# Kernel tuning notes

Measured on AMD Instinct MI355X. Metric: run time of the kernel, lower is better.

## Reference

```python
import jax, jax.numpy as jnp
import numpy as np
import math

# dims (match init_kwargs / input_specs)
T, B, S = 2048, 8, 512
D, H, DFF, NQ, W = 512, 8, 2048, 10, 16
EPS = 1e-5
NEG = -1e30


def _ln(x, g, b):
    mu = jnp.mean(x, axis=-1, keepdims=True)
    var = jnp.mean((x - mu) ** 2, axis=-1, keepdims=True)
    return (x - mu) * jax.lax.rsqrt(var + EPS) * g + b


def setup_inputs() -> dict:
    key = jax.random.key(0)
    ks = jax.random.split(key, 10)
    f = lambda k, shape, s=0.02: jax.random.normal(k, shape, jnp.float32) * s
    return {
        'tgt': jax.random.normal(ks[0], (T, B, D), jnp.float32),
        'memory': jax.random.normal(ks[1], (S, B, D), jnp.float32),
        'queries': f(ks[2], (NQ, D), 1.0 / math.sqrt(D)),
        'wk': f(ks[3], (NQ, 1), 1.0 / math.sqrt(NQ)),
        'in_proj_w': f(ks[4], (3 * D, D)),
        'in_proj_b': jnp.zeros((3 * D,), jnp.float32),
        'out_proj_w': f(ks[5], (D, D)),
        'out_proj_b': jnp.zeros((D,), jnp.float32),
        'lin1_w': f(ks[6], (DFF, D)),
        'lin1_b': jnp.zeros((DFF,), jnp.float32),
        'lin2_w': f(ks[7], (D, DFF)),
        'lin2_b': jnp.zeros((D,), jnp.float32),
        'ln1_g': jnp.ones((D,), jnp.float32), 'ln1_b': jnp.zeros((D,), jnp.float32),
        'ln2_g': jnp.ones((D,), jnp.float32), 'ln2_b': jnp.zeros((D,), jnp.float32),
        'ln3_g': jnp.ones((D,), jnp.float32), 'ln3_b': jnp.zeros((D,), jnp.float32),
    }


def _qa_block(x, queries, wk):
    # x: (T, B, D). Learned queries: per-head unit-norm + depth scale (QaN).
    dh = D // H
    q = queries.reshape(NQ, H, dh)
    q = q / (jnp.linalg.norm(q, axis=-1, keepdims=True) + 1e-6)
    q = (q / math.sqrt(dh)).reshape(NQ, D)
    # LocalAttention(window=W, look_backward=1, look_forward=1, non-causal, autopad)
    # k = v = x; T % W == 0 so autopad is a no-op.
    xb = jnp.transpose(x, (1, 0, 2))                       # (B, T, D)
    nw = T // W
    scale = D ** -0.5                                      # dim_head = D (single-head local attn)
    bk = xb.reshape(B, nw, W, D)
    pad = jnp.zeros((B, 1, W, D), x.dtype)
    bkp = jnp.concatenate([pad, bk, pad], axis=1)          # (B, nw+2, W, D)
    kv = jnp.concatenate([bkp[:, i:i + nw] for i in range(3)], axis=2)  # (B, nw, 3W, D)
    win_ok = jnp.pad(jnp.ones((nw,), bool), (1, 1))
    vm = jnp.stack([win_ok[i:i + nw] for i in range(3)], axis=1)        # (nw, 3)
    kmask = jnp.repeat(vm, W, axis=1)                                   # (nw, 3W)
    # The query vector is identical for every time step, so every position in a
    # window sees the same (query, keyset) pair -> one attention row per (n, window).
    sim = jnp.einsum('nd,bmjd->bnmj', q * scale, kv)       # (B, NQ, nw, 3W)
    sim = jnp.where(kmask[None, None], sim, NEG)
    attn = jax.nn.softmax(sim, axis=-1)
    out = jnp.einsum('bnmj,bmjd->bnmd', attn, kv)          # (B, NQ, nw, D)
    out = jnp.einsum('bnmd,n->bmd', out, wk[:, 0])         # mix N queries via wk (N,1)
    out = jnp.broadcast_to(out[:, :, None], (B, nw, W, D)).reshape(B, T, D)
    return jnp.transpose(out, (1, 0, 2))                   # (T, B, D)


def _mha_block(x, mem, in_w, in_b, out_w, out_b):
    dh = D // H
    wq, wkk, wv = jnp.split(in_w, 3, axis=0)
    bq, bk, bv = jnp.split(in_b, 3)
    q = (x @ wq.T + bq).reshape(T, B, H, dh).transpose(1, 2, 0, 3)   # (B,H,T,dh)
    k = (mem @ wkk.T + bk).reshape(S, B, H, dh).transpose(1, 2, 0, 3)
    v = (mem @ wv.T + bv).reshape(S, B, H, dh).transpose(1, 2, 0, 3)
    attn = jax.nn.softmax(jnp.einsum('bhtd,bhsd->bhts', q, k) / math.sqrt(dh), axis=-1)
    o = jnp.einsum('bhts,bhsd->bhtd', attn, v).transpose(2, 0, 1, 3).reshape(T, B, D)
    return o @ out_w.T + out_b


def reference(tgt, memory, queries, wk, in_proj_w, in_proj_b, out_proj_w, out_proj_b,
              lin1_w, lin1_b, lin2_w, lin2_b, ln1_g, ln1_b, ln2_g, ln2_b, ln3_g, ln3_b):
    # post-norm (norm_first=False), eval mode: dropouts + stochastic_depth(rate=0) are identity
    x = tgt
    x = _ln(x + _qa_block(x, queries, wk), ln1_g, ln1_b)
    x = _ln(x + _mha_block(x, memory, in_proj_w, in_proj_b, out_proj_w, out_proj_b), ln2_g, ln2_b)
    ff = jax.nn.relu(x @ lin1_w.T + lin1_b) @ lin2_w.T + lin2_b
    x = _ln(x + ff, ln3_g, ln3_b)
    # x = tgt + stochastic_depth(x - tgt) == x in eval / rate 0
    return x
```

## Files before the change

### kernel.cpp

```cpp
#include <hip/hip_runtime.h>


typedef unsigned short u16;
typedef unsigned int u32;
typedef short short8_t __attribute__((ext_vector_type(8)));
typedef float f32x4 __attribute__((ext_vector_type(4)));

#define TT 2048
#define BB 8
#define SS 512
#define DD 512
#define HH 8
#define DH 64
#define DFF 2048
#define NQ 10
#define WW 16
#define NW 128
#define KVPART 2097152

__device__ __forceinline__ float b2f(u16 u) {
    return __uint_as_float(((unsigned int)u) << 16);
}
__device__ __forceinline__ u16 f2b(float f) {
    unsigned int x = __float_as_uint(f);
    unsigned int r = x + 0x7FFFu + ((x >> 16) & 1u);
    return (u16)(r >> 16);
}
__device__ __forceinline__ u32 cvt_pk_bf16(float lo, float hi) {
    u32 r;
    asm volatile("v_cvt_pk_bf16_f32 %0, %1, %2" : "=v"(r) : "v"(lo), "v"(hi));
    return r;
}
__device__ __forceinline__ float wave_sum(float v) {
    #pragma unroll
    for (int o = 32; o > 0; o >>= 1) v += __shfl_xor(v, o, 64);
    return v;
}
__device__ __forceinline__ float wave_max(float v) {
    #pragma unroll
    for (int o = 32; o > 0; o >>= 1) v = fmaxf(v, __shfl_xor(v, o, 64));
    return v;
}
__device__ __forceinline__ void load4(const u16* p, float* v) {
    ushort4 t = *(const ushort4*)p;
    v[0] = b2f(t.x); v[1] = b2f(t.y); v[2] = b2f(t.z); v[3] = b2f(t.w);
}
__device__ __forceinline__ void load4(const float* p, float* v) {
    float4 t = *(const float4*)p;
    v[0] = t.x; v[1] = t.y; v[2] = t.z; v[3] = t.w;
}
__device__ __forceinline__ void st1(u16* p, float v) { *p = f2b(v); }
__device__ __forceinline__ void st1(float* p, float v) { *p = v; }

__device__ __forceinline__ void async16(const u16* g, u16* l) {
    __builtin_amdgcn_global_load_lds((const __attribute__((address_space(1))) u32*)g,
                                     (__attribute__((address_space(3))) u32*)l, 16, 0, 0);
}

__device__ __forceinline__ void xcd_remap(int& bx, int& by) {
    int flat = blockIdx.y * gridDim.x + blockIdx.x;
    int xcd = flat & 7;
    int j = flat >> 3;
    by = xcd * ((int)gridDim.y >> 3) + j / (int)gridDim.x;
    bx = j % (int)gridDim.x;
}

__device__ __forceinline__ void cvt_block(const float* s, u16* d, int base) {
    int i = base + threadIdx.x * 4;
    float4 v = *(const float4*)(s + i);
    ushort4 o;
    o.x = f2b(v.x); o.y = f2b(v.y); o.z = f2b(v.z); o.w = f2b(v.w);
    *(ushort4*)(d + i) = o;
}

__global__ __launch_bounds__(256) void cvt2_kernel(const float* __restrict__ s0,
                                                   const float* __restrict__ s1,
                                                   u16* __restrict__ d0,
                                                   u16* __restrict__ d1) {
    int bid = blockIdx.x;
    if (bid < 2048) cvt_block(s0, d0, bid * 1024);
    else            cvt_block(s1, d1, (bid - 2048) * 1024);
}

__global__ __launch_bounds__(256) void cvt3_kernel(const float* __restrict__ s0,
                                                   const float* __restrict__ s1,
                                                   const float* __restrict__ s2,
                                                   u16* __restrict__ d0,
                                                   u16* __restrict__ d1,
                                                   u16* __restrict__ d2) {
    int bid = blockIdx.x;
    if (bid < 256)       cvt_block(s0, d0, bid * 1024);
    else if (bid < 1280) cvt_block(s1, d1, (bid - 256) * 1024);
    else                 cvt_block(s2, d2, (bid - 1280) * 1024);
}

__global__ __launch_bounds__(512) void qeff_kernel(const float* __restrict__ queries,
                                                   float* __restrict__ qeff) {
    int d = threadIdx.x;
    const float KS = 0.0055242717280199026f;
    for (int n = 0; n < NQ; n++) {
        float v = queries[n * DD + d];
        float ss = wave_sum(v * v);
        float norm = sqrtf(ss);
        qeff[n * DD + d] = v / (norm + 1e-6f) * KS;
    }
}

__global__ __launch_bounds__(256) void p_kernel(const float* __restrict__ x,
                                                const float* __restrict__ qeff,
                                                float* __restrict__ p) {
    __shared__ float qe[NQ * DD];
    for (int i = threadIdx.x; i < NQ * DD; i += 256) qe[i] = qeff[i];
    __syncthreads();
    int b = blockIdx.x >> 9;
    int t = ((blockIdx.x & 511) << 2) + (threadIdx.x >> 6);
    int lane = threadIdx.x & 63;
    const float* xr = x + ((size_t)t * BB + b) * DD;
    float acc[NQ];
    #pragma unroll
    for (int n = 0; n < NQ; n++) acc[n] = 0.f;
    #pragma unroll
    for (int c = 0; c < 8; c++) {
        int d = c * 64 + lane;
        float xv = xr[d];
        #pragma unroll
        for (int n = 0; n < NQ; n++) acc[n] += xv * qe[n * DD + d];
    }
    #pragma unroll
    for (int n = 0; n < NQ; n++) {
        float s = wave_sum(acc[n]);
        if (lane == 0) p[((size_t)(b * NQ + n)) * TT + t] = s;
    }
}

__global__ __launch_bounds__(256) void winmix_kernel(const float* __restrict__ p,
                                                     const float* __restrict__ wk,
                                                     const float* __restrict__ x,
                                                     float* __restrict__ mixed) {
    __shared__ float As[48];
    int id = blockIdx.x;
    int b = id >> 7, m = id & 127;
    if (threadIdx.x < 64) {
        int j = threadIdx.x;
        int tj = (m - 1) * WW + j;
        bool valid = (j < 48) && (tj >= 0) && (tj < TT);
        float acc = 0.f;
        for (int n = 0; n < NQ; n++) {
            float v = valid ? p[((size_t)(b * NQ + n)) * TT + tj] : -1e30f;
            float mx = wave_max(v);
            float e = valid ? __expf(v - mx) : 0.f;
            float s = wave_sum(e);
            acc += wk[n] * (e / s);
        }
        if (j < 48) As[j] = acc;
    }
    __syncthreads();
    int d0 = threadIdx.x, d1 = threadIdx.x + 256;
    float a0 = 0.f, a1 = 0.f;
    int tb = (m - 1) * WW;
    for (int j = 0; j < 48; j++) {
        int t = tb + j;
        if ((unsigned)t < (unsigned)TT) {
            float aj = As[j];
            const float* xr = x + ((size_t)t * BB + b) * DD;
            a0 += aj * xr[d0];
            a1 += aj * xr[d1];
        }
    }
    mixed[(size_t)id * DD + d0] = a0;
    mixed[(size_t)id * DD + d1] = a1;
}

__global__ __launch_bounds__(256) void ln_qa_kernel(const float* __restrict__ a,
                                                    const float* __restrict__ mixed,
                                                    const float* __restrict__ g,
                                                    const float* __restrict__ bt,
                                                    u16* __restrict__ out) {
    int r = blockIdx.x * 4 + (threadIdx.x >> 6);
    int lane = threadIdx.x & 63;
    int t = r >> 3, b = r & 7;
    const float* ar = a + (size_t)r * DD;
    const float* mr = mixed + ((size_t)(b * NW + (t >> 4))) * DD;
    int d0 = lane * 8;
    float av[8], mv[8], gg[8], bb[8];
    load4(ar + d0, av); load4(ar + d0 + 4, av + 4);
    load4(mr + d0, mv); load4(mr + d0 + 4, mv + 4);
    load4(g + d0, gg);  load4(g + d0 + 4, gg + 4);
    load4(bt + d0, bb); load4(bt + d0 + 4, bb + 4);
    float v[8];
    float s = 0.f, s2 = 0.f;
    #pragma unroll
    for (int u = 0; u < 8; u++) { v[u] = av[u] + mv[u]; s += v[u]; s2 += v[u] * v[u]; }
    s = wave_sum(s); s2 = wave_sum(s2);
    float mu = s * (1.f / DD);
    float var = s2 * (1.f / DD) - mu * mu;
    float rs = rsqrtf(var + 1e-5f);
    #pragma unroll
    for (int u = 0; u < 8; u++) out[(size_t)r * DD + d0 + u] = f2b((v[u] - mu) * rs * gg[u] + bb[u]);
}

template <typename OT>
__global__ __launch_bounds__(256) void ln_rows_kernel(const u16* __restrict__ a,
                                                      const u16* __restrict__ bsrc,
                                                      const float* __restrict__ g,
                                                      const float* __restrict__ bt,
                                                      OT* __restrict__ out) {
    int r = blockIdx.x * 4 + (threadIdx.x >> 6);
    int lane = threadIdx.x & 63;
    const u16* ar = a + (size_t)r * DD;
    const u16* br = bsrc + (size_t)r * DD;
    int d0 = lane * 8;
    float av[8], cv[8], gg[8], bb[8];
    load4(ar + d0, av); load4(ar + d0 + 4, av + 4);
    load4(br + d0, cv); load4(br + d0 + 4, cv + 4);
    load4(g + d0, gg);  load4(g + d0 + 4, gg + 4);
    load4(bt + d0, bb); load4(bt + d0 + 4, bb + 4);
    float v[8];
    float s = 0.f, s2 = 0.f;
    #pragma unroll
    for (int u = 0; u < 8; u++) { v[u] = av[u] + cv[u]; s += v[u]; s2 += v[u] * v[u]; }
    s = wave_sum(s); s2 = wave_sum(s2);
    float mu = s * (1.f / DD);
    float var = s2 * (1.f / DD) - mu * mu;
    float rs = rsqrtf(var + 1e-5f);
    #pragma unroll
    for (int u = 0; u < 8; u++) st1(out + (size_t)r * DD + d0 + u, (v[u] - mu) * rs * gg[u] + bb[u]);
}

template <int RELU, int MT, int KV>
__global__ __launch_bounds__(256) void gemm_lds(const u16* __restrict__ A,
                                                const u16* __restrict__ W,
                                                const float* __restrict__ bias,
                                                u16* __restrict__ C,
                                                int M, int N, int K) {
    constexpr int BM = MT * 32;
    constexpr int NIA = BM / 64;
    __shared__ u16 As[2][BM * 32];
    __shared__ u16 Bs[2][128 * 32];
    int tid = threadIdx.x;
    int w = tid >> 6, lane = tid & 63;
    int n16 = lane & 15, quad = lane >> 4;
    int m0 = blockIdx.y * BM, n0 = blockIdx.x * 128;
    int wm16 = (w >> 1) * MT;
    int wn = (w & 1) * 64;

    const u16* gA[NIA];
    u16* lA[NIA];
    #pragma unroll
    for (int i = 0; i < NIA; i++) {
        int s = (w * NIA + i) * 64 + lane;
        int mb = s >> 6, kseg = (s >> 4) & 3, m = s & 15;
        gA[i] = A + (size_t)(m0 + mb * 16 + m) * K + kseg * 8;
        lA[i] = &As[0][(size_t)((w * NIA + i) * 64) * 8];
    }
    const u16* gB[2];
    u16* lB[2];
    #pragma unroll
    for (int i = 0; i < 2; i++) {
        int s = (w * 2 + i) * 64 + lane;
        int nb = s >> 6, kseg = (s >> 4) & 3, n = s & 15;
        gB[i] = W + (size_t)(n0 + nb * 16 + n) * K + kseg * 8;
        lB[i] = &Bs[0][(size_t)((w * 2 + i) * 64) * 8];
    }

    f32x4 acc[MT][4];
    #pragma unroll
    for (int i = 0; i < MT; i++)
        #pragma unroll
        for (int j = 0; j < 4; j++) acc[i][j] = (f32x4){0.f, 0.f, 0.f, 0.f};

    const int nk = K >> 5;
    #pragma unroll
    for (int i = 0; i < NIA; i++) async16(gA[i], lA[i]);
    #pragma unroll
    for (int i = 0; i < 2; i++) async16(gB[i], lB[i]);
    __syncthreads();

    for (int t = 0; t < nk; t++) {
        int cur = t & 1;
        if (t + 1 < nk) {
            int nxt = cur ^ 1;
            #pragma unroll
            for (int i = 0; i < NIA; i++) async16(gA[i] + (t + 1) * 32, lA[i] + nxt * (BM * 32));
            #pragma unroll
            for (int i = 0; i < 2; i++) async16(gB[i] + (t + 1) * 32, lB[i] + nxt * 4096);
        }
        const u16* Ac = &As[cur][0];
        const u16* Bc = &Bs[cur][0];
        short8_t af[MT], bf[4];
        #pragma unroll
        for (int im = 0; im < MT; im++)
            af[im] = *(const short8_t*)(Ac + (size_t)((wm16 + im) * 64 + lane) * 8);
        #pragma unroll
        for (int in = 0; in < 4; in++)
            bf[in] = *(const short8_t*)(Bc + (size_t)(((w & 1) * 4 + in) * 64 + lane) * 8);
        #pragma unroll
        for (int im = 0; im < MT; im++)
            #pragma unroll
            for (int in = 0; in < 4; in++)
                acc[im][in] = __builtin_amdgcn_mfma_f32_16x16x32_bf16(af[im], bf[in], acc[im][in], 0, 0, 0);
        __syncthreads();
    }

    float bia[4];
    #pragma unroll
    for (int in = 0; in < 4; in++) bia[in] = bias[n0 + wn + in * 16 + n16];
    #pragma unroll
    for (int im = 0; im < MT; im++) {
        #pragma unroll
        for (int r = 0; r < 4; r++) {
            int row = m0 + (wm16 + im) * 16 + quad * 4 + r;
            #pragma unroll
            for (int in = 0; in < 4; in++) {
                float v = acc[im][in][r] + bia[in];
                if (RELU) v = fmaxf(v, 0.f);
                if (KV) {
                    int col = n0 + wn + in * 16 + n16;
                    int part = col >> 9, h = (col >> 6) & 7, d = col & 63;
                    int s = row >> 3, bq = row & 7;
                    C[(size_t)part * KVPART + ((size_t)(bq * HH + h) * SS + s) * DH + d] = f2b(v);
                } else {
                    C[(size_t)row * N + n0 + wn + in * 16 + n16] = f2b(v);
                }
            }
        }
    }
}

template <int RELU, int KV>
__global__ __launch_bounds__(256) void gemm_np(const u16* __restrict__ A,
                                               const u16* __restrict__ W,
                                               const float* __restrict__ bias,
                                               u16* __restrict__ C,
                                               int M, int N, int K) {
    __shared__ u16 As[3][64 * 32];
    __shared__ u16 Bs[3][64 * 32];
    int tid = threadIdx.x;
    int w = tid >> 6, lane = tid & 63;
    int n16 = lane & 15, quad = lane >> 4;
    int bx, by;
    xcd_remap(bx, by);
    int m0 = by * 64, n0 = bx * 64;
    int wm16 = (w >> 1) * 2;
    int wn = (w & 1) * 32;

    const u16* gA0 = A + (size_t)(m0 + w * 16 + n16) * K + quad * 8;
    const u16* gB0 = W + (size_t)(n0 + w * 16 + n16) * K + quad * 8;

    f32x4 acc[2][2];
    #pragma unroll
    for (int i = 0; i < 2; i++)
        #pragma unroll
        for (int j = 0; j < 2; j++) acc[i][j] = (f32x4){0.f, 0.f, 0.f, 0.f};

    const int nk = K >> 5;
    async16(gA0, &As[0][w * 512]);
    async16(gB0, &Bs[0][w * 512]);
    async16(gA0 + 32, &As[1][w * 512]);
    async16(gB0 + 32, &Bs[1][w * 512]);

    int cur = 0;
    for (int t = 0; t < nk; t++) {
        if (t + 1 < nk) {
            __asm__ volatile("s_waitcnt vmcnt(2)" ::: "memory");
        } else {
            __asm__ volatile("s_waitcnt vmcnt(0)" ::: "memory");
        }
        __builtin_amdgcn_s_barrier();
        __builtin_amdgcn_sched_barrier(0);
        if (t + 2 < nk) {
            int nx2 = cur + 2; if (nx2 >= 3) nx2 -= 3;
            async16(gA0 + (t + 2) * 32, &As[nx2][w * 512]);
            async16(gB0 + (t + 2) * 32, &Bs[nx2][w * 512]);
        }
        const u16* Ac = &As[cur][0];
        const u16* Bc = &Bs[cur][0];
        short8_t af[2], bf[2];
        #pragma unroll
        for (int im = 0; im < 2; im++)
            af[im] = *(const short8_t*)(Ac + (size_t)((wm16 + im) * 64 + lane) * 8);
        #pragma unroll
        for (int in = 0; in < 2; in++)
            bf[in] = *(const short8_t*)(Bc + (size_t)(((w & 1) * 2 + in) * 64 + lane) * 8);
        #pragma unroll
        for (int im = 0; im < 2; im++)
            #pragma unroll
            for (int in = 0; in < 2; in++)
                acc[im][in] = __builtin_amdgcn_mfma_f32_16x16x32_bf16(af[im], bf[in], acc[im][in], 0, 0, 0);
        __asm__ volatile("s_waitcnt lgkmcnt(0)" ::: "memory");
        cur = (cur == 2) ? 0 : cur + 1;
    }

    float bia[2];
    #pragma unroll
    for (int in = 0; in < 2; in++) bia[in] = bias[n0 + wn + in * 16 + n16];
    #pragma unroll
    for (int im = 0; im < 2; im++) {
        #pragma unroll
        for (int r = 0; r < 4; r++) {
            int row = m0 + (wm16 + im) * 16 + quad * 4 + r;
            #pragma unroll
            for (int in = 0; in < 2; in++) {
                float v = acc[im][in][r] + bia[in];
                if (RELU) v = fmaxf(v, 0.f);
                if (KV) {
                    int col = n0 + wn + in * 16 + n16;
                    int part = col >> 9, h = (col >> 6) & 7, d = col & 63;
                    int s = row >> 3, bq = row & 7;
                    C[(size_t)part * KVPART + ((size_t)(bq * HH + h) * SS + s) * DH + d] = f2b(v);
                } else {
                    C[(size_t)row * N + n0 + wn + in * 16 + n16] = f2b(v);
                }
            }
        }
    }
}

__global__ __launch_bounds__(256, 1) void ffn_fused(const u16* __restrict__ A,
                                                    const u16* __restrict__ W1,
                                                    const float* __restrict__ b1,
                                                    const u16* __restrict__ W2,
                                                    const float* __restrict__ b2,
                                                    u16* __restrict__ Cout) {
    __shared__ u16 W1b[2][32 * 512];
    __shared__ u16 Vt[2][512][40];
    __shared__ float b1s[DFF];
    int tid = threadIdx.x;
    int w = tid >> 6, lane = tid & 63;
    int n16 = lane & 15, quad = lane >> 4, q8 = quad * 8;
    int m0 = blockIdx.x * 64;
    int row = m0 + w * 16 + n16;

    for (int i = tid; i < DFF; i += 256) b1s[i] = b1[i];

    short8_t aq[16];
    {
        const u16* ar = A + (size_t)row * DD + q8;
        #pragma unroll
        for (int ks = 0; ks < 16; ks++)
            aq[ks] = *(const short8_t*)(ar + ks * 32);
    }

    const u16* gW1 = W1 + (size_t)((w >> 1) * 16 + n16) * DD + ((w & 1) * 8) * 32 + q8;
    int h4 = (tid & 7) * 4;
    int pos = (h4 < 16) ? ((h4 >> 2) << 3) : ((((h4 - 16) >> 2) << 3) + 4);
    const u16* gW2 = W2 + (size_t)(tid >> 3) * DFF + h4;

    f32x4 acc[32];
    #pragma unroll
    for (int ot = 0; ot < 32; ot++) acc[ot] = (f32x4){0.f, 0.f, 0.f, 0.f};

    union PU { u32 wd[4]; short8_t s8; };

    #pragma unroll
    for (int i = 0; i < 8; i++)
        async16(gW1 + i * 32, &W1b[0][(size_t)(w * 8 + i) * 512]);
    #pragma unroll
    for (int i = 0; i < 16; i++) {
        ushort4 v = *(const ushort4*)(gW2 + (size_t)i * 32 * DFF);
        *(ushort4*)&Vt[0][i * 32 + (tid >> 3)][pos] = v;
    }
    __syncthreads();

    for (int c = 0; c < 64; c++) {
        int cur = c & 1, nxt = cur ^ 1;

        ushort4 w2r[16];
        if (c < 63) {
            const u16* gW2c = gW2 + (size_t)(c + 1) * 32;
            #pragma unroll
            for (int i = 0; i < 16; i++)
                w2r[i] = *(const ushort4*)(gW2c + (size_t)i * 32 * DFF);
            const u16* gW1c = gW1 + (size_t)(c + 1) * 32 * DD;
            #pragma unroll
            for (int i = 0; i < 8; i++)
                async16(gW1c + i * 32, &W1b[nxt][(size_t)(w * 8 + i) * 512]);
        }

        f32x4 s0 = (f32x4){0.f, 0.f, 0.f, 0.f};
        f32x4 s1 = (f32x4){0.f, 0.f, 0.f, 0.f};
        #pragma unroll
        for (int ks = 0; ks < 16; ks++) {
            short8_t f0 = *(const short8_t*)&W1b[cur][(size_t)ks * 512 + lane * 8];
            s0 = __builtin_amdgcn_mfma_f32_16x16x32_bf16(f0, aq[ks], s0, 0, 0, 0);
        }
        #pragma unroll
        for (int ks = 0; ks < 16; ks++) {
            short8_t f1 = *(const short8_t*)&W1b[cur][(size_t)(16 + ks) * 512 + lane * 8];
            s1 = __builtin_amdgcn_mfma_f32_16x16x32_bf16(f1, aq[ks], s1, 0, 0, 0);
        }

        float p0 = fmaxf(s0[0] + b1s[c * 32 + quad * 4 + 0], 0.f);
        float p1 = fmaxf(s0[1] + b1s[c * 32 + quad * 4 + 1], 0.f);
        float p2 = fmaxf(s0[2] + b1s[c * 32 + quad * 4 + 2], 0.f);
        float p3 = fmaxf(s0[3] + b1s[c * 32 + quad * 4 + 3], 0.f);
        float p4 = fmaxf(s1[0] + b1s[c * 32 + 16 + quad * 4 + 0], 0.f);
        float p5 = fmaxf(s1[1] + b1s[c * 32 + 16 + quad * 4 + 1], 0.f);
        float p6 = fmaxf(s1[2] + b1s[c * 32 + 16 + quad * 4 + 2], 0.f);
        float p7 = fmaxf(s1[3] + b1s[c * 32 + 16 + quad * 4 + 3], 0.f);

        PU pu;
        pu.wd[0] = cvt_pk_bf16(p0, p1);
        pu.wd[1] = cvt_pk_bf16(p2, p3);
        pu.wd[2] = cvt_pk_bf16(p4, p5);
        pu.wd[3] = cvt_pk_bf16(p6, p7);

        #pragma unroll
        for (int ot = 0; ot < 32; ot++) {
            short8_t bv = *(const short8_t*)&Vt[cur][ot * 16 + n16][q8];
            acc[ot] = __builtin_amdgcn_mfma_f32_16x16x32_bf16(pu.s8, bv, acc[ot], 0, 0, 0);
        }

        if (c < 63) {
            #pragma unroll
            for (int i = 0; i < 16; i++)
                *(ushort4*)&Vt[nxt][i * 32 + (tid >> 3)][pos] = w2r[i];
        }
        __syncthreads();
    }

    #pragma unroll
    for (int ot = 0; ot < 32; ot++) {
        float bia = b2[ot * 16 + n16];
        #pragma unroll
        for (int r = 0; r < 4; r++) {
            int ro = m0 + w * 16 + quad * 4 + r;
            Cout[(size_t)ro * DD + ot * 16 + n16] = f2b(acc[ot][r] + bia);
        }
    }
}

__global__ __launch_bounds__(256) void attn_wp(const u16* __restrict__ qb,
                                               const u16* __restrict__ kvb,
                                               u16* __restrict__ ob) {
    __shared__ u16 Kb[2][2048];
    __shared__ u16 Vt[2][64][40];
    int tid = threadIdx.x;
    int w = tid >> 6, lane = tid & 63;
    int n16 = lane & 15, quad = lane >> 4, q8 = quad * 8;
    int xb, bh;
    xcd_remap(xb, bh);
    int b = bh >> 3, h = bh & 7;
    int q0 = xb * 128 + w * 32;

    short8_t aq[2][2];
    #pragma unroll
    for (int qt = 0; qt < 2; qt++) {
        const u16* qrow = qb + ((size_t)(q0 + qt * 16 + n16) * BB + b) * DD + h * DH;
        aq[qt][0] = *(const short8_t*)(qrow + q8);
        aq[qt][1] = *(const short8_t*)(qrow + 32 + q8);
    }

    const u16* kbase = kvb + (size_t)(b * HH + h) * (SS * DH);
    const u16* vbase = kvb + (size_t)KVPART + (size_t)(b * HH + h) * (SS * DH);

    const u16* gK = kbase + (size_t)((w >> 1) * 16 + n16) * DH + (w & 1) * 32 + q8;

    int m = lane & 15;
    int a2 = m >> 2, b2 = m & 3;
    int key0 = (b2 < 2) ? (4 * a2 + 2 * b2) : (16 + 4 * a2 + 2 * (b2 - 2));
    int kp2 = m * 2;
    int vd = w * 16 + quad * 4;
    const u16* gV = vbase + (size_t)key0 * DH + vd;

    float lsum[2] = {0.f, 0.f};
    f32x4 Oa[2][4];
    #pragma unroll
    for (int qt = 0; qt < 2; qt++)
        #pragma unroll
        for (int ot = 0; ot < 4; ot++) Oa[qt][ot] = (f32x4){0.f, 0.f, 0.f, 0.f};

    union VU { ushort4 q; u16 h[4]; };
    union PU { u32 wd[4]; short8_t s8; };

    {
        async16(gK, &Kb[0][w * 512]);
        VU va, vb2;
        va.q  = *(const ushort4*)(gV);
        vb2.q = *(const ushort4*)(gV + DH);
        #pragma unroll
        for (int u = 0; u < 4; u++)
            *(u32*)&Vt[0][vd + u][kp2] = (u32)va.h[u] | ((u32)vb2.h[u] << 16);
    }
    __syncthreads();

    for (int c = 0; c < 16; c++) {
        int cur = c & 1, nxt = cur ^ 1;

        VU va, vb2;
        if (c < 15) {
            const u16* gVc = gV + (size_t)(c + 1) * 32 * DH;
            va.q  = *(const ushort4*)(gVc);
            vb2.q = *(const ushort4*)(gVc + DH);
            async16(gK + (size_t)(c + 1) * 32 * DH, &Kb[nxt][w * 512]);
        }

        short8_t bk0 = *(const short8_t*)&Kb[cur][0 * 512 + lane * 8];
        short8_t bk1 = *(const short8_t*)&Kb[cur][1 * 512 + lane * 8];
        short8_t bk2 = *(const short8_t*)&Kb[cur][2 * 512 + lane * 8];
        short8_t bk3 = *(const short8_t*)&Kb[cur][3 * 512 + lane * 8];

        #pragma unroll
        for (int qt = 0; qt < 2; qt++) {
            f32x4 s0 = (f32x4){0.f, 0.f, 0.f, 0.f};
            s0 = __builtin_amdgcn_mfma_f32_16x16x32_bf16(bk0, aq[qt][0], s0, 0, 0, 0);
            s0 = __builtin_amdgcn_mfma_f32_16x16x32_bf16(bk1, aq[qt][1], s0, 0, 0, 0);
            f32x4 s1 = (f32x4){0.f, 0.f, 0.f, 0.f};
            s1 = __builtin_amdgcn_mfma_f32_16x16x32_bf16(bk2, aq[qt][0], s1, 0, 0, 0);
            s1 = __builtin_amdgcn_mfma_f32_16x16x32_bf16(bk3, aq[qt][1], s1, 0, 0, 0);

            float p0 = __expf(s0[0] * 0.125f - 8.0f);
            float p1 = __expf(s0[1] * 0.125f - 8.0f);
            float p2 = __expf(s0[2] * 0.125f - 8.0f);
            float p3 = __expf(s0[3] * 0.125f - 8.0f);
            float p4 = __expf(s1[0] * 0.125f - 8.0f);
            float p5 = __expf(s1[1] * 0.125f - 8.0f);
            float p6 = __expf(s1[2] * 0.125f - 8.0f);
            float p7 = __expf(s1[3] * 0.125f - 8.0f);
            lsum[qt] += ((p0 + p1) + (p2 + p3)) + ((p4 + p5) + (p6 + p7));

            PU pu;
            pu.wd[0] = cvt_pk_bf16(p0, p1);
            pu.wd[1] = cvt_pk_bf16(p2, p3);
            pu.wd[2] = cvt_pk_bf16(p4, p5);
            pu.wd[3] = cvt_pk_bf16(p6, p7);

            #pragma unroll
            for (int ot = 0; ot < 4; ot++) {
                short8_t bv = *(const short8_t*)&Vt[cur][ot * 16 + n16][q8];
                Oa[qt][ot] = __builtin_amdgcn_mfma_f32_16x16x32_bf16(pu.s8, bv, Oa[qt][ot], 0, 0, 0);
            }
        }

        if (c < 15) {
            #pragma unroll
            for (int u = 0; u < 4; u++)
                *(u32*)&Vt[nxt][vd + u][kp2] = (u32)va.h[u] | ((u32)vb2.h[u] << 16);
        }
        __syncthreads();
    }

    #pragma unroll
    for (int qt = 0; qt < 2; qt++) {
        float l = lsum[qt];
        l += __shfl_xor(l, 16, 64);
        l += __shfl_xor(l, 32, 64);
        #pragma unroll
        for (int r = 0; r < 4; r++) {
            float lq = __shfl(l, quad * 4 + r, 64);
            float inv = 1.f / lq;
            int t = q0 + qt * 16 + quad * 4 + r;
            u16* orow = ob + ((size_t)t * BB + b) * DD + h * DH + n16;
            #pragma unroll
            for (int ot = 0; ot < 4; ot++) orow[ot * 16] = f2b(Oa[qt][ot][r] * inv);
        }
    }
}

extern "C" void kernel_launch(void* const* d_in, const int* in_sizes, int n_in,
                              void* d_out, int out_size, void* d_ws, size_t ws_size,
                              hipStream_t stream) {
    const float* tgt       = (const float*)d_in[0];
    const float* memory    = (const float*)d_in[1];
    const float* queries   = (const float*)d_in[2];
    const float* wk        = (const float*)d_in[3];
    const float* in_proj_w = (const float*)d_in[4];
    const float* in_proj_b = (const float*)d_in[5];
    const float* out_proj_w= (const float*)d_in[6];
    const float* out_proj_b= (const float*)d_in[7];
    const float* lin1_w    = (const float*)d_in[8];
    const float* lin1_b    = (const float*)d_in[9];
    const float* lin2_w    = (const float*)d_in[10];
    const float* lin2_b    = (const float*)d_in[11];
    const float* ln1_g     = (const float*)d_in[12];
    const float* ln1_b     = (const float*)d_in[13];
    const float* ln2_g     = (const float*)d_in[14];
    const float* ln2_b     = (const float*)d_in[15];
    const float* ln3_g     = (const float*)d_in[16];
    const float* ln3_b     = (const float*)d_in[17];

    char* w = (char*)d_ws;
    float* qeff  = (float*)(w + 0);
    float* pbuf  = (float*)(w + 20480);
    float* mixed = (float*)(w + 872448);
    u16* y1  = (u16*)(w + 2969600);
    u16* qb  = (u16*)(w + 19746816);
    u16* kvb = (u16*)(w + 36524032);
    u16* ob  = (u16*)(w + 44912640);
    u16* ipwb = (u16*)(w + 44912640);
    u16* memb = (u16*)(w + 46485504);
    u16* opwb = (u16*)(w + 36524032);
    u16* l1wb = (u16*)(w + 37048320);
    u16* l2wb = (u16*)(w + 39145472);
    u16* t1 = qb;
    u16* y2 = ob;
    u16* fb = y1;

    cvt2_kernel<<<2816, 256, 0, stream>>>(memory, in_proj_w, memb, ipwb);

    qeff_kernel<<<1, 512, 0, stream>>>(queries, qeff);
    p_kernel<<<BB * (TT / 4), 256, 0, stream>>>(tgt, qeff, pbuf);
    winmix_kernel<<<BB * NW, 256, 0, stream>>>(pbuf, wk, tgt, mixed);
    ln_qa_kernel<<<(TT * BB) / 4, 256, 0, stream>>>(tgt, mixed, ln1_g, ln1_b, y1);

    gemm_lds<0, 4, 0><<<dim3(DD / 128, (TT * BB) / 128), 256, 0, stream>>>(y1, ipwb, in_proj_b, qb, TT * BB, DD, DD);
    gemm_np<0, 1><<<dim3(1024 / 64, (SS * BB) / 64), 256, 0, stream>>>(memb, ipwb + (size_t)DD * DD, in_proj_b + DD, kvb, SS * BB, 1024, DD);
    attn_wp<<<dim3(TT / 128, BB * HH), 256, 0, stream>>>(qb, kvb, ob);
    cvt3_kernel<<<2304, 256, 0, stream>>>(out_proj_w, lin1_w, lin2_w, opwb, l1wb, l2wb);
    gemm_lds<0, 4, 0><<<dim3(DD / 128, (TT * BB) / 128), 256, 0, stream>>>(ob, opwb, out_proj_b, t1, TT * BB, DD, DD);
    ln_rows_kernel<u16><<<(TT * BB) / 4, 256, 0, stream>>>(y1, t1, ln2_g, ln2_b, y2);

    ffn_fused<<<(TT * BB) / 64, 256, 0, stream>>>(y2, l1wb, lin1_b, l2wb, lin2_b, fb);
    ln_rows_kernel<float><<<(TT * BB) / 4, 256, 0, stream>>>(y2, fb, ln3_g, ln3_b, (float*)d_out);
}
```

Measured before the change: 472.8 us.

## Pre-swizzle lin2 weights into MFMA fragment order and async-load in FFN

The conversion kernel now writes lin2_w to bf16 in the exact per-lane MFMA fragment order the FFN kernel consumes, instead of a plain row-major copy. The fused FFN kernel can then stream W2 chunks with async 16-byte global-to-LDS copies, the same way it already loads W1. This replaces the register-staged ushort4 gathers and scattered LDS writes and removes the padded transposed buffer. The conversion grid also shrinks because each thread handles eight elements.

```diff
diff --git a/kernel.cpp b/kernel.cpp
--- a/kernel.cpp
+++ b/kernel.cpp
@@ -89,9 +89,25 @@
                                                    u16* __restrict__ d1,
                                                    u16* __restrict__ d2) {
     int bid = blockIdx.x;
-    if (bid < 256)       cvt_block(s0, d0, bid * 1024);
-    else if (bid < 1280) cvt_block(s1, d1, (bid - 256) * 1024);
-    else                 cvt_block(s2, d2, (bid - 1280) * 1024);
+    if (bid < 256) {
+        cvt_block(s0, d0, bid * 1024);
+    } else if (bid < 1280) {
+        cvt_block(s1, d1, (bid - 256) * 1024);
+    } else {
+        int g = (bid - 1280) * 256 + threadIdx.x;
+        int l = g & 63, ot = (g >> 6) & 31, c = g >> 11;
+        int quad = l >> 4;
+        int o = ot * 16 + (l & 15);
+        const float* src = s2 + (size_t)o * DFF + c * 32 + 4 * quad;
+        float4 v0 = *(const float4*)(src);
+        float4 v1 = *(const float4*)(src + 16);
+        ushort4 o0, o1;
+        o0.x = f2b(v0.x); o0.y = f2b(v0.y); o0.z = f2b(v0.z); o0.w = f2b(v0.w);
+        o1.x = f2b(v1.x); o1.y = f2b(v1.y); o1.z = f2b(v1.z); o1.w = f2b(v1.w);
+        u16* dst = d2 + (size_t)g * 8;
+        *(ushort4*)(dst) = o0;
+        *(ushort4*)(dst + 4) = o1;
+    }
 }
 
 __global__ __launch_bounds__(512) void qeff_kernel(const float* __restrict__ queries,
@@ -419,11 +435,11 @@
 __global__ __launch_bounds__(256, 1) void ffn_fused(const u16* __restrict__ A,
                                                     const u16* __restrict__ W1,
                                                     const float* __restrict__ b1,
-                                                    const u16* __restrict__ W2,
+                                                    const u16* __restrict__ W2s,
                                                     const float* __restrict__ b2,
                                                     u16* __restrict__ Cout) {
     __shared__ u16 W1b[2][32 * 512];
-    __shared__ u16 Vt[2][512][40];
+    __shared__ u16 W2b[2][32 * 512];
     __shared__ float b1s[DFF];
     int tid = threadIdx.x;
     int w = tid >> 6, lane = tid & 63;
@@ -442,9 +458,7 @@
     }
 
     const u16* gW1 = W1 + (size_t)((w >> 1) * 16 + n16) * DD + ((w & 1) * 8) * 32 + q8;
-    int h4 = (tid & 7) * 4;
-    int pos = (h4 < 16) ? ((h4 >> 2) << 3) : ((((h4 - 16) >> 2) << 3) + 4);
-    const u16* gW2 = W2 + (size_t)(tid >> 3) * DFF + h4;
+    const u16* gW2 = W2s + (size_t)(w * 8) * 512 + lane * 8;
 
     f32x4 acc[32];
     #pragma unroll
@@ -453,28 +467,23 @@
     union PU { u32 wd[4]; short8_t s8; };
 
     #pragma unroll
-    for (int i = 0; i < 8; i++)
+    for (int i = 0; i < 8; i++) {
         async16(gW1 + i * 32, &W1b[0][(size_t)(w * 8 + i) * 512]);
-    #pragma unroll
-    for (int i = 0; i < 16; i++) {
-        ushort4 v = *(const ushort4*)(gW2 + (size_t)i * 32 * DFF);
-        *(ushort4*)&Vt[0][i * 32 + (tid >> 3)][pos] = v;
+        async16(gW2 + i * 512, &W2b[0][(size_t)(w * 8 + i) * 512]);
     }
     __syncthreads();
 
     for (int c = 0; c < 64; c++) {
         int cur = c & 1, nxt = cur ^ 1;
 
-        ushort4 w2r[16];
         if (c < 63) {
-            const u16* gW2c = gW2 + (size_t)(c + 1) * 32;
-            #pragma unroll
-            for (int i = 0; i < 16; i++)
-                w2r[i] = *(const ushort4*)(gW2c + (size_t)i * 32 * DFF);
             const u16* gW1c = gW1 + (size_t)(c + 1) * 32 * DD;
-            #pragma unroll
-            for (int i = 0; i < 8; i++)
+            const u16* gW2c = gW2 + (size_t)(c + 1) * 16384;
+            #pragma unroll
+            for (int i = 0; i < 8; i++) {
                 async16(gW1c + i * 32, &W1b[nxt][(size_t)(w * 8 + i) * 512]);
+                async16(gW2c + i * 512, &W2b[nxt][(size_t)(w * 8 + i) * 512]);
+            }
         }
 
         f32x4 s0 = (f32x4){0.f, 0.f, 0.f, 0.f};
@@ -507,15 +516,10 @@
 
         #pragma unroll
         for (int ot = 0; ot < 32; ot++) {
-            short8_t bv = *(const short8_t*)&Vt[cur][ot * 16 + n16][q8];
+            short8_t bv = *(const short8_t*)&W2b[cur][(size_t)ot * 512 + lane * 8];
             acc[ot] = __builtin_amdgcn_mfma_f32_16x16x32_bf16(pu.s8, bv, acc[ot], 0, 0, 0);
         }
 
-        if (c < 63) {
-            #pragma unroll
-            for (int i = 0; i < 16; i++)
-                *(ushort4*)&Vt[nxt][i * 32 + (tid >> 3)][pos] = w2r[i];
-        }
         __syncthreads();
     }
 
@@ -689,9 +693,9 @@
     u16* ob  = (u16*)(w + 44912640);
     u16* ipwb = (u16*)(w + 44912640);
     u16* memb = (u16*)(w + 46485504);
-    u16* opwb = (u16*)(w + 36524032);
-    u16* l1wb = (u16*)(w + 37048320);
-    u16* l2wb = (u16*)(w + 39145472);
+    u16* opwb  = (u16*)(w + 36524032);
+    u16* l1wb  = (u16*)(w + 37048320);
+    u16* l2sig = (u16*)(w + 39145472);
     u16* t1 = qb;
     u16* y2 = ob;
     u16* fb = y1;
@@ -706,10 +710,10 @@
     gemm_lds<0, 4, 0><<<dim3(DD / 128, (TT * BB) / 128), 256, 0, stream>>>(y1, ipwb, in_proj_b, qb, TT * BB, DD, DD);
     gemm_np<0, 1><<<dim3(1024 / 64, (SS * BB) / 64), 256, 0, stream>>>(memb, ipwb + (size_t)DD * DD, in_proj_b + DD, kvb, SS * BB, 1024, DD);
     attn_wp<<<dim3(TT / 128, BB * HH), 256, 0, stream>>>(qb, kvb, ob);
-    cvt3_kernel<<<2304, 256, 0, stream>>>(out_proj_w, lin1_w, lin2_w, opwb, l1wb, l2wb);
+    cvt3_kernel<<<1792, 256, 0, stream>>>(out_proj_w, lin1_w, lin2_w, opwb, l1wb, l2sig);
     gemm_lds<0, 4, 0><<<dim3(DD / 128, (TT * BB) / 128), 256, 0, stream>>>(ob, opwb, out_proj_b, t1, TT * BB, DD, DD);
     ln_rows_kernel<u16><<<(TT * BB) / 4, 256, 0, stream>>>(y1, t1, ln2_g, ln2_b, y2);
 
-    ffn_fused<<<(TT * BB) / 64, 256, 0, stream>>>(y2, l1wb, lin1_b, l2wb, lin2_b, fb);
+    ffn_fused<<<(TT * BB) / 64, 256, 0, stream>>>(y2, l1wb, lin1_b, l2sig, lin2_b, fb);
     ln_rows_kernel<float><<<(TT * BB) / 4, 256, 0, stream>>>(y2, fb, ln3_g, ln3_b, (float*)d_out);
 }
```

Measured after the change: 473.5 us. About the same (+0.1%).
